# Optimization experiments

Measured on AMD Instinct MI355X. Metric: run time of the kernel, lower is better.

## Reference

```python
import jax, jax.numpy as jnp
import numpy as np

SP, WD, H, HID = 8, 3, 8, 256
D = HID // H
TEMP = 0.1


def setup_inputs() -> dict:
    key = jax.random.key(0)
    ks = jax.random.split(key, 14)
    B, Lq, Lk, F = 4, 1024, 2048, SP + WD
    s = 0.05
    return {
        "q_fp": jax.random.normal(ks[0], (B, Lq, F), jnp.float32),
        "v_ret": jax.random.normal(ks[1], (B, Lk, F), jnp.float32),
        "pi_star": jax.random.uniform(ks[2], (B, Lq, Lk), jnp.float32),
        "Wq_s": jax.random.normal(ks[3], (HID, SP), jnp.float32) * s,
        "bq_s": jax.random.normal(ks[4], (HID,), jnp.float32) * s,
        "Wk_s": jax.random.normal(ks[5], (HID, SP), jnp.float32) * s,
        "bk_s": jax.random.normal(ks[6], (HID,), jnp.float32) * s,
        "Wq_w": jax.random.normal(ks[7], (HID, WD), jnp.float32) * s,
        "bq_w": jax.random.normal(ks[8], (HID,), jnp.float32) * s,
        "Wk_w": jax.random.normal(ks[9], (HID, WD), jnp.float32) * s,
        "bk_w": jax.random.normal(ks[10], (HID,), jnp.float32) * s,
        "Wv": jax.random.normal(ks[11], (HID, F), jnp.float32) * s,
        "bv": jnp.zeros((HID,), jnp.float32),
        "Wo": jax.random.normal(ks[12], (HID, HID), jnp.float32) * s,
        "bo": jnp.zeros((HID,), jnp.float32),
        "wave_blend": jnp.array(0.5, jnp.float32),
    }


def _proj(x, W, b):
    # x: [B, L, F_in] -> [B, H, L, D]
    B, L, _ = x.shape
    return (x @ W.T + b).reshape(B, L, H, D).transpose(0, 2, 1, 3)


def reference(q_fp, v_ret, pi_star, Wq_s, bq_s, Wk_s, bk_s, Wq_w, bq_w, Wk_w, bk_w, Wv, bv, Wo, bo, wave_blend):
    B, Lq, _ = q_fp.shape
    # split streams: first SP dims spatial, next WD dims wave (F == SP+WD)
    q_sp, q_wv = q_fp[..., :SP], q_fp[..., SP:SP + WD]
    k_sp, k_wv = v_ret[..., :SP], v_ret[..., SP:SP + WD]
    # structural branch: scaled dot product
    q_struct = _proj(q_sp, Wq_s, bq_s)
    k_struct = _proj(k_sp, Wk_s, bk_s)
    spatial_logits = jnp.einsum('bhqd,bhkd->bhqk', q_struct, k_struct) / np.float32(np.sqrt(D))
    # wave branch: negative squared euclidean distance via norm expansion
    q_wp = _proj(q_wv, Wq_w, bq_w)
    k_wp = _proj(k_wv, Wk_w, bk_w)
    qn = jnp.sum(q_wp * q_wp, axis=-1)[..., :, None]   # [B,H,Lq,1]
    kn = jnp.sum(k_wp * k_wp, axis=-1)[..., None, :]   # [B,H,1,Lk]
    qk = jnp.einsum('bhqd,bhkd->bhqk', q_wp, k_wp)
    wave_logits = -(qn + kn - 2.0 * qk) / np.float32(TEMP)
    alpha = jax.nn.sigmoid(wave_blend)
    transport_mask = jnp.log(jnp.clip(pi_star, 1e-9, None))[:, None]  # [B,1,Lq,Lk]
    attn = jax.nn.softmax((1.0 - alpha) * spatial_logits + alpha * wave_logits + transport_mask, axis=-1)
    values = _proj(v_ret, Wv, bv)  # [B,H,Lk,D]
    ctx = jnp.einsum('bhqk,bhkd->bhqd', attn, values)
    ctx = ctx.transpose(0, 2, 1, 3).reshape(B, Lq, HID)
    return ctx @ Wo.T + bo
```

## Files before the change

kernel.cpp:

```cpp
#include <hip/hip_runtime.h>
#include <hip/hip_bf16.h>
#include <cstdint>

#define B_    4
#define LQ    1024
#define LK    2048
#define FEAT  11
#define SP_   8
#define WD_   3
#define H_    8
#define HID_  256
#define LOG2E 1.4426950408889634f
#define SPLIT 2
#define KPS   (LK / SPLIT)
#define ITERS (KPS / 64)

typedef __attribute__((ext_vector_type(4))) float f32x4;
typedef __attribute__((ext_vector_type(8))) short bf16x8;
typedef __attribute__((ext_vector_type(4))) short s16x4;

__device__ __forceinline__ float sigmoidf_(float x) { return 1.f / (1.f + __expf(-x)); }

__device__ __forceinline__ short f2bf(float f) {
  unsigned u = __float_as_uint(f);
  u += 0x7fffu + ((u >> 16) & 1u);
  return (short)(u >> 16);
}
__device__ __forceinline__ float bf2f(short s) {
  return __uint_as_float(((unsigned)(unsigned short)s) << 16);
}

__device__ __forceinline__ void gl_lds16(const void* g, void* l) {
  __builtin_amdgcn_global_load_lds(
      (const __attribute__((address_space(1))) unsigned int*)g,
      (__attribute__((address_space(3))) unsigned int*)l, 16, 0, 0);
}

__global__ __launch_bounds__(256) void proj_q_kernel(
    const float* __restrict__ q_fp, const float* __restrict__ Wq_s,
    const float* __restrict__ bq_s, const float* __restrict__ Wq_w,
    const float* __restrict__ bq_w, const float* __restrict__ wb,
    short* __restrict__ Qh)
{
  const int row = blockIdx.x;
  const int t   = threadIdx.x;
  const float alpha = sigmoidf_(wb[0]);
  const float c1 = (1.f - alpha) * 0.17677669529663687f * LOG2E;
  const float c2 = 2.f * alpha * 10.f * LOG2E;

  const float* x = q_fp + (size_t)row * FEAT;
  float xs[FEAT];
  #pragma unroll
  for (int f = 0; f < FEAT; ++f) xs[f] = x[f];

  float s = bq_s[t];
  #pragma unroll
  for (int f = 0; f < SP_; ++f) s += xs[f] * Wq_s[t * SP_ + f];
  float w = bq_w[t];
  #pragma unroll
  for (int f = 0; f < WD_; ++f) w += xs[SP_ + f] * Wq_w[t * WD_ + f];

  const int h = t >> 5, d = t & 31;
  const int b = row >> 10, q = row & (LQ - 1);
  const size_t base = ((size_t)(b * H_ + h) * LQ + q) * 64;
  Qh[base + d]      = f2bf(c1 * s);
  Qh[base + 32 + d] = f2bf(c2 * w);
}

__global__ __launch_bounds__(256) void projk_pack_kernel(
    const float* __restrict__ v_ret, const float* __restrict__ Wk_s,
    const float* __restrict__ bk_s, const float* __restrict__ Wk_w,
    const float* __restrict__ bk_w, const float* __restrict__ Wv,
    const float* __restrict__ bv,   const float* __restrict__ wb,
    short* __restrict__ KV, float* __restrict__ kb)
{
  __shared__ float ldsv[64][33];
  const int blk = blockIdx.x, bh = blockIdx.y;
  const int b = bh >> 3, h = bh & 7;
  const int t = threadIdx.x;
  const int kl = t >> 2, part = t & 3;
  const int k = blk * 64 + kl;
  const float alpha = sigmoidf_(wb[0]);

  const float* x = v_ret + (size_t)(b * LK + k) * FEAT;
  float xs[FEAT];
  #pragma unroll
  for (int f = 0; f < FEAT; ++f) xs[f] = x[f];

  float s8[8], w8[8], v8[8];
  #pragma unroll
  for (int i = 0; i < 8; ++i) {
    const int d = h * 32 + part * 8 + i;
    float s = bk_s[d];
    #pragma unroll
    for (int f = 0; f < SP_; ++f) s += xs[f] * Wk_s[d * SP_ + f];
    float w = bk_w[d];
    #pragma unroll
    for (int f = 0; f < WD_; ++f) w += xs[SP_ + f] * Wk_w[d * WD_ + f];
    float v = bv[d];
    #pragma unroll
    for (int f = 0; f < FEAT; ++f) v += xs[f] * Wv[d * FEAT + f];
    s8[i] = s; w8[i] = w; v8[i] = v;
    ldsv[kl][part * 8 + i] = v;
  }

  float sq = 0.f;
  #pragma unroll
  for (int i = 0; i < 8; ++i) sq += w8[i] * w8[i];
  sq += __shfl_xor(sq, 1);
  sq += __shfl_xor(sq, 2);
  if (part == 0) kb[(size_t)bh * LK + k] = -10.f * alpha * LOG2E * sq;

  const int a  = kl >> 5;
  const int bb = (kl >> 2) & 1;
  const int p  = kl - a * 32 - bb * 4;
  const int lo = ((p >> 3) << 2) | (p & 3);
  const int t4 = a * 2 + bb;
  const size_t base = ((size_t)bh * 32 + blk) * 768;

  bf16x8 hs, hw;
  #pragma unroll
  for (int i = 0; i < 8; ++i) { hs[i] = f2bf(s8[i]); hw[i] = f2bf(w8[i]); }
  *(bf16x8*)(KV + (base + (t4 * 2 + 0) * 64 + part * 16 + lo) * 8) = hs;
  *(bf16x8*)(KV + (base + (t4 * 2 + 1) * 64 + part * 16 + lo) * 8) = hw;

  __syncthreads();

  {
    const int j = t >> 6, l = t & 63;
    const int dt = j >> 1, kw = j & 1;
    const int lo2 = l & 15, quad = l >> 4;
    const int d = dt * 16 + lo2;
    bf16x8 hv;
    #pragma unroll
    for (int i = 0; i < 8; ++i)
      hv[i] = f2bf(ldsv[kw * 32 + quad * 8 + i][d]);
    *(bf16x8*)(KV + (base + 512 + t) * 8) = hv;
  }
}

__global__ __launch_bounds__(256) void pi_prepack_kernel(
    const float* __restrict__ pi, float* __restrict__ piP)
{
  const int Gid = blockIdx.x * 256 + threadIdx.x;
  const int g    = Gid & 255;
  const int kblk = (Gid >> 8) & 31;
  const int qt   = (Gid >> 13) & 63;
  const int b    = Gid >> 19;
  const int t4 = g >> 6, l = g & 63;
  const int lo = l & 15, quad = l >> 4;
  const int q = qt * 16 + lo;
  const int k = kblk * 64 + ((t4 >> 1) << 5) + ((t4 & 1) << 2) + quad * 8;
  const f32x4 v = *(const f32x4*)(pi + ((size_t)(b * LQ + q) * LK + k));
  *(f32x4*)(piP + (size_t)Gid * 4) = v;
}

union PF { int i[4]; bf16x8 v; };

__global__ __launch_bounds__(256, 4) void attn_kernel(
    const short* __restrict__ Qh, const short* __restrict__ KV,
    const float* __restrict__ kb, const float* __restrict__ piP,
    float* __restrict__ part)
{
  __shared__ short skv[2][6144];
  const int bh = blockIdx.y;
  const int sp = blockIdx.z;
  const int b = bh >> 3;
  const int wv = threadIdx.x >> 6;
  const int lane = threadIdx.x & 63;
  const int lo16 = lane & 15;
  const int quad = lane >> 4;
  const int q = blockIdx.x * 64 + wv * 16 + lo16;
  const int qt = blockIdx.x * 4 + wv;
  const int k0 = sp * KPS;
  const int blk0 = sp * 16;

  const size_t qoff = ((size_t)bh * LQ + q) * 64 + quad * 8;
  const bf16x8 qh0 = *(const bf16x8*)(Qh + qoff);
  const bf16x8 qh1 = *(const bf16x8*)(Qh + qoff + 32);

  const float* pibase = piP + (((size_t)(b * 64 + qt) * 32 + blk0) << 10) + lane * 4;
  const float* kbbase = kb + (size_t)bh * LK + k0 + quad * 8;

  float m = -1e30f, l = 0.f;
  f32x4 o0 = {0.f, 0.f, 0.f, 0.f}, o1 = {0.f, 0.f, 0.f, 0.f};

  {
    const size_t gb = ((size_t)bh * 32 + blk0) * 768;
    #pragma unroll
    for (int c = 0; c < 3; ++c)
      gl_lds16(KV + (gb + c * 256 + wv * 64 + lane) * 8,
               &skv[0][c * 2048 + wv * 512]);
  }

  #pragma unroll 2
  for (int it = 0; it < ITERS; ++it) {
    __syncthreads();
    if (it + 1 < ITERS) {
      const size_t gb = ((size_t)bh * 32 + blk0 + it + 1) * 768;
      short* db = skv[(it + 1) & 1];
      #pragma unroll
      for (int c = 0; c < 3; ++c)
        gl_lds16(KV + (gb + c * 256 + wv * 64 + lane) * 8,
                 db + c * 2048 + wv * 512);
    }
    const short* cbuf = skv[it & 1];

    const float* pp = pibase + (it << 10);
    f32x4 pi4[4];
    #pragma unroll
    for (int t4 = 0; t4 < 4; ++t4) pi4[t4] = *(const f32x4*)(pp + t4 * 256);
    const float* bp = kbbase + it * 64;
    f32x4 kb4[4];
    kb4[0] = *(const f32x4*)(bp);      kb4[1] = *(const f32x4*)(bp + 4);
    kb4[2] = *(const f32x4*)(bp + 32); kb4[3] = *(const f32x4*)(bp + 36);

    f32x4 st[4];
    #pragma unroll
    for (int t4 = 0; t4 < 4; ++t4) {
      const bf16x8 ka0 = *(const bf16x8*)(cbuf + ((t4 * 2 + 0) * 64 + lane) * 8);
      const bf16x8 ka1 = *(const bf16x8*)(cbuf + ((t4 * 2 + 1) * 64 + lane) * 8);
      f32x4 z = {0.f, 0.f, 0.f, 0.f};
      z = __builtin_amdgcn_mfma_f32_16x16x32_bf16(ka0, qh0, z, 0, 0, 0);
      z = __builtin_amdgcn_mfma_f32_16x16x32_bf16(ka1, qh1, z, 0, 0, 0);
      st[t4] = z;
    }

    float lg[16];
    #pragma unroll
    for (int t4 = 0; t4 < 4; ++t4) {
      #pragma unroll
      for (int r = 0; r < 4; ++r) lg[t4 * 4 + r] = st[t4][r] + kb4[t4][r];
    }

    float cm = lg[0];
    #pragma unroll
    for (int j = 1; j < 16; ++j) cm = fmaxf(cm, lg[j]);
    cm = fmaxf(cm, __shfl_xor(cm, 16));
    cm = fmaxf(cm, __shfl_xor(cm, 32));
    const float mn = fmaxf(m, cm);
    const float sc = __builtin_amdgcn_exp2f(m - mn);

    unsigned eu[16];
    #pragma unroll
    for (int t4 = 0; t4 < 4; ++t4) {
      #pragma unroll
      for (int r = 0; r < 4; ++r)
        eu[t4 * 4 + r] = __float_as_uint(
            __builtin_amdgcn_exp2f(lg[t4 * 4 + r] - mn) * fmaxf(pi4[t4][r], 1e-9f));
    }

    PF pf0, pf1;
    float ps = 0.f;
    #pragma unroll
    for (int p = 0; p < 4; ++p) {
      const int w0 = __builtin_amdgcn_perm(eu[2 * p + 1], eu[2 * p], 0x07060302u);
      const int w1 = __builtin_amdgcn_perm(eu[8 + 2 * p + 1], eu[8 + 2 * p], 0x07060302u);
      pf0.i[p] = w0; pf1.i[p] = w1;
      ps += __uint_as_float(((unsigned)w0) << 16) + __uint_as_float(w0 & 0xffff0000u);
      ps += __uint_as_float(((unsigned)w1) << 16) + __uint_as_float(w1 & 0xffff0000u);
    }
    ps += __shfl_xor(ps, 16);
    ps += __shfl_xor(ps, 32);
    l = l * sc + ps;
    m = mn;
    #pragma unroll
    for (int r = 0; r < 4; ++r) { o0[r] *= sc; o1[r] *= sc; }

    const bf16x8 va00 = *(const bf16x8*)(cbuf + ((512 + 0 * 64) + lane) * 8);
    const bf16x8 va01 = *(const bf16x8*)(cbuf + ((512 + 1 * 64) + lane) * 8);
    const bf16x8 va10 = *(const bf16x8*)(cbuf + ((512 + 2 * 64) + lane) * 8);
    const bf16x8 va11 = *(const bf16x8*)(cbuf + ((512 + 3 * 64) + lane) * 8);
    o0 = __builtin_amdgcn_mfma_f32_16x16x32_bf16(va00, pf0.v, o0, 0, 0, 0);
    o0 = __builtin_amdgcn_mfma_f32_16x16x32_bf16(va01, pf1.v, o0, 0, 0, 0);
    o1 = __builtin_amdgcn_mfma_f32_16x16x32_bf16(va10, pf0.v, o1, 0, 0, 0);
    o1 = __builtin_amdgcn_mfma_f32_16x16x32_bf16(va11, pf1.v, o1, 0, 0, 0);
  }

  float* ppart = part + ((size_t)(sp * 32 + bh) * LQ + q) * 36;
  if (quad == 0) { ppart[0] = m; ppart[1] = l; }
  *(f32x4*)(ppart + 4 + quad * 4)  = o0;
  *(f32x4*)(ppart + 20 + quad * 4) = o1;
}

__global__ __launch_bounds__(256) void wo_prep_kernel(
    const float* __restrict__ Wo, short* __restrict__ WoH, short* __restrict__ WoL)
{
  const int i = (blockIdx.x * 256 + threadIdx.x) * 4;
  const f32x4 v = *(const f32x4*)(Wo + i);
  s16x4 h, l;
  #pragma unroll
  for (int j = 0; j < 4; ++j) {
    h[j] = f2bf(v[j]);
    l[j] = f2bf(v[j] - bf2f(h[j]));
  }
  *(s16x4*)(WoH + i) = h;
  *(s16x4*)(WoL + i) = l;
}

__global__ __launch_bounds__(256) void out_kernel(
    const float* __restrict__ part, const short* __restrict__ WoH,
    const short* __restrict__ WoL, const float* __restrict__ bo,
    float* __restrict__ out)
{
  const int t = threadIdx.x;
  const int wv = t >> 6, lane = t & 63;
  const int lo16 = lane & 15, quad = lane >> 4;
  const int mt = blockIdx.x;
  const size_t gq = (size_t)mt * 16 + lo16;
  const int b = (int)(gq >> 10), qq = (int)(gq & (LQ - 1));

  bf16x8 Ah[8], Al[8];
  #pragma unroll
  for (int win = 0; win < 8; ++win) {
    const size_t r = (size_t)(b * H_ + win) * LQ + qq;
    const float* p0 = part + r * 36;
    const float* p1 = part + (r + (size_t)B_ * H_ * LQ) * 36;
    const float m0 = p0[0], l0 = p0[1], m1 = p1[0], l1 = p1[1];
    const float mM = fmaxf(m0, m1);
    const float w0 = __builtin_amdgcn_exp2f(m0 - mM);
    const float w1 = __builtin_amdgcn_exp2f(m1 - mM);
    const float inv = 1.f / (w0 * l0 + w1 * l1);
    const f32x4 a0  = *(const f32x4*)(p0 + 4 + quad * 8);
    const f32x4 a0b = *(const f32x4*)(p0 + 8 + quad * 8);
    const f32x4 a1  = *(const f32x4*)(p1 + 4 + quad * 8);
    const f32x4 a1b = *(const f32x4*)(p1 + 8 + quad * 8);
    float c8[8];
    #pragma unroll
    for (int j = 0; j < 4; ++j) {
      c8[j]     = (w0 * a0[j]  + w1 * a1[j])  * inv;
      c8[4 + j] = (w0 * a0b[j] + w1 * a1b[j]) * inv;
    }
    #pragma unroll
    for (int j = 0; j < 8; ++j) {
      const short hi = f2bf(c8[j]);
      Ah[win][j] = hi;
      Al[win][j] = f2bf(c8[j] - bf2f(hi));
    }
  }

  const int n0 = wv * 64;
  #pragma unroll
  for (int nt = 0; nt < 4; ++nt) {
    const int nb = n0 + nt * 16;
    const short* bh = WoH + (size_t)(nb + lo16) * HID_ + quad * 8;
    const short* bl = WoL + (size_t)(nb + lo16) * HID_ + quad * 8;
    const float bias = bo[nb + lo16];
    f32x4 acc = {bias, bias, bias, bias};
    #pragma unroll
    for (int win = 0; win < 8; ++win) {
      const bf16x8 Bh = *(const bf16x8*)(bh + win * 32);
      const bf16x8 Bl = *(const bf16x8*)(bl + win * 32);
      acc = __builtin_amdgcn_mfma_f32_16x16x32_bf16(Ah[win], Bh, acc, 0, 0, 0);
      acc = __builtin_amdgcn_mfma_f32_16x16x32_bf16(Al[win], Bh, acc, 0, 0, 0);
      acc = __builtin_amdgcn_mfma_f32_16x16x32_bf16(Ah[win], Bl, acc, 0, 0, 0);
    }
    #pragma unroll
    for (int r4 = 0; r4 < 4; ++r4)
      out[(size_t)(mt * 16 + quad * 4 + r4) * HID_ + nb + lo16] = acc[r4];
  }
}

extern "C" void kernel_launch(void* const* d_in, const int* in_sizes, int n_in,
                              void* d_out, int out_size, void* d_ws, size_t ws_size,
                              hipStream_t stream)
{
  const float* q_fp  = (const float*)d_in[0];
  const float* v_ret = (const float*)d_in[1];
  const float* pi    = (const float*)d_in[2];
  const float* Wq_s  = (const float*)d_in[3];
  const float* bq_s  = (const float*)d_in[4];
  const float* Wk_s  = (const float*)d_in[5];
  const float* bk_s  = (const float*)d_in[6];
  const float* Wq_w  = (const float*)d_in[7];
  const float* bq_w  = (const float*)d_in[8];
  const float* Wk_w  = (const float*)d_in[9];
  const float* bk_w  = (const float*)d_in[10];
  const float* Wv    = (const float*)d_in[11];
  const float* bv    = (const float*)d_in[12];
  const float* Wo    = (const float*)d_in[13];
  const float* bo    = (const float*)d_in[14];
  const float* wb    = (const float*)d_in[15];
  float* out = (float*)d_out;

  short* Qh   = (short*)d_ws;
  short* KV   = Qh + (size_t)2097152;
  float* kbuf = (float*)(KV + (size_t)6291456);
  float* piP  = kbuf + (size_t)65536;
  float* part = piP + (size_t)8388608;
  short* WoH  = (short*)piP;
  short* WoL  = WoH + (size_t)65536;

  proj_q_kernel<<<B_ * LQ, 256, 0, stream>>>(q_fp, Wq_s, bq_s, Wq_w, bq_w, wb, Qh);
  projk_pack_kernel<<<dim3(LK / 64, 32), 256, 0, stream>>>(
      v_ret, Wk_s, bk_s, Wk_w, bk_w, Wv, bv, wb, KV, kbuf);
  pi_prepack_kernel<<<8192, 256, 0, stream>>>(pi, piP);
  attn_kernel<<<dim3(LQ / 64, 32, SPLIT), 256, 0, stream>>>(Qh, KV, kbuf, piP, part);
  wo_prep_kernel<<<64, 256, 0, stream>>>(Wo, WoH, WoL);
  out_kernel<<<(B_ * LQ) / 16, 256, 0, stream>>>(part, WoH, WoL, bo, out);
}
```

Measured before the change: 179.1 us.

## Software-pipeline pi/kb loads with manual double-buffer unroll and remap grid to 1D

Restructures the attention loop into an explicit two-stage unroll: pi and key-bias values for the next step are loaded into registers while the current step computes, and LDS buffers are addressed statically. The grid becomes 1D with batch-head and split interleaved in the low bits of the block id, changing block scheduling order. The clamp on pi before multiplying is removed. Register pressure rises from the extra prefetched vectors, which may affect occupancy.

```diff
diff --git a/kernel.cpp b/kernel.cpp
--- a/kernel.cpp
+++ b/kernel.cpp
@@ -157,22 +157,91 @@
 
 union PF { int i[4]; bf16x8 v; };
 
+__device__ __forceinline__ void attn_step(
+    const short* __restrict__ cbuf, bf16x8 qh0, bf16x8 qh1,
+    const f32x4* __restrict__ pi4, const f32x4* __restrict__ kb4,
+    int lane, float& m, float& l, f32x4& o0, f32x4& o1)
+{
+  f32x4 st[4];
+  #pragma unroll
+  for (int t4 = 0; t4 < 4; ++t4) {
+    const bf16x8 ka0 = *(const bf16x8*)(cbuf + ((t4 * 2 + 0) * 64 + lane) * 8);
+    const bf16x8 ka1 = *(const bf16x8*)(cbuf + ((t4 * 2 + 1) * 64 + lane) * 8);
+    f32x4 z = {0.f, 0.f, 0.f, 0.f};
+    z = __builtin_amdgcn_mfma_f32_16x16x32_bf16(ka0, qh0, z, 0, 0, 0);
+    z = __builtin_amdgcn_mfma_f32_16x16x32_bf16(ka1, qh1, z, 0, 0, 0);
+    st[t4] = z;
+  }
+
+  float lg[16];
+  #pragma unroll
+  for (int t4 = 0; t4 < 4; ++t4) {
+    #pragma unroll
+    for (int r = 0; r < 4; ++r) lg[t4 * 4 + r] = st[t4][r] + kb4[t4][r];
+  }
+
+  float cm = lg[0];
+  #pragma unroll
+  for (int j = 1; j < 16; ++j) cm = fmaxf(cm, lg[j]);
+  cm = fmaxf(cm, __shfl_xor(cm, 16));
+  cm = fmaxf(cm, __shfl_xor(cm, 32));
+  const float mn = fmaxf(m, cm);
+  const float sc = __builtin_amdgcn_exp2f(m - mn);
+
+  unsigned eu[16];
+  #pragma unroll
+  for (int t4 = 0; t4 < 4; ++t4) {
+    #pragma unroll
+    for (int r = 0; r < 4; ++r)
+      eu[t4 * 4 + r] = __float_as_uint(
+          __builtin_amdgcn_exp2f(lg[t4 * 4 + r] - mn) * pi4[t4][r]);
+  }
+
+  PF pf0, pf1;
+  float ps = 0.f;
+  #pragma unroll
+  for (int p = 0; p < 4; ++p) {
+    const int w0 = __builtin_amdgcn_perm(eu[2 * p + 1], eu[2 * p], 0x07060302u);
+    const int w1 = __builtin_amdgcn_perm(eu[8 + 2 * p + 1], eu[8 + 2 * p], 0x07060302u);
+    pf0.i[p] = w0; pf1.i[p] = w1;
+    ps += __uint_as_float(((unsigned)w0) << 16) + __uint_as_float(w0 & 0xffff0000u);
+    ps += __uint_as_float(((unsigned)w1) << 16) + __uint_as_float(w1 & 0xffff0000u);
+  }
+  ps += __shfl_xor(ps, 16);
+  ps += __shfl_xor(ps, 32);
+  l = l * sc + ps;
+  m = mn;
+  #pragma unroll
+  for (int r = 0; r < 4; ++r) { o0[r] *= sc; o1[r] *= sc; }
+
+  const bf16x8 va00 = *(const bf16x8*)(cbuf + ((512 + 0 * 64) + lane) * 8);
+  const bf16x8 va01 = *(const bf16x8*)(cbuf + ((512 + 1 * 64) + lane) * 8);
+  const bf16x8 va10 = *(const bf16x8*)(cbuf + ((512 + 2 * 64) + lane) * 8);
+  const bf16x8 va11 = *(const bf16x8*)(cbuf + ((512 + 3 * 64) + lane) * 8);
+  o0 = __builtin_amdgcn_mfma_f32_16x16x32_bf16(va00, pf0.v, o0, 0, 0, 0);
+  o0 = __builtin_amdgcn_mfma_f32_16x16x32_bf16(va01, pf1.v, o0, 0, 0, 0);
+  o1 = __builtin_amdgcn_mfma_f32_16x16x32_bf16(va10, pf0.v, o1, 0, 0, 0);
+  o1 = __builtin_amdgcn_mfma_f32_16x16x32_bf16(va11, pf1.v, o1, 0, 0, 0);
+}
+
 __global__ __launch_bounds__(256, 4) void attn_kernel(
     const short* __restrict__ Qh, const short* __restrict__ KV,
     const float* __restrict__ kb, const float* __restrict__ piP,
     float* __restrict__ part)
 {
   __shared__ short skv[2][6144];
-  const int bh = blockIdx.y;
-  const int sp = blockIdx.z;
+  const int id = blockIdx.x;
+  const int combo = id & 63;
+  const int qblk  = id >> 6;
+  const int bh = combo >> 1;
+  const int sp = combo & 1;
   const int b = bh >> 3;
   const int wv = threadIdx.x >> 6;
   const int lane = threadIdx.x & 63;
   const int lo16 = lane & 15;
   const int quad = lane >> 4;
-  const int q = blockIdx.x * 64 + wv * 16 + lo16;
-  const int qt = blockIdx.x * 4 + wv;
-  const int k0 = sp * KPS;
+  const int q  = qblk * 64 + wv * 16 + lo16;
+  const int qt = qblk * 4 + wv;
   const int blk0 = sp * 16;
 
   const size_t qoff = ((size_t)bh * LQ + q) * 64 + quad * 8;
@@ -180,7 +249,7 @@
   const bf16x8 qh1 = *(const bf16x8*)(Qh + qoff + 32);
 
   const float* pibase = piP + (((size_t)(b * 64 + qt) * 32 + blk0) << 10) + lane * 4;
-  const float* kbbase = kb + (size_t)bh * LK + k0 + quad * 8;
+  const float* kbbase = kb + (size_t)bh * LK + sp * KPS + quad * 8;
 
   float m = -1e30f, l = 0.f;
   f32x4 o0 = {0.f, 0.f, 0.f, 0.f}, o1 = {0.f, 0.f, 0.f, 0.f};
@@ -193,89 +262,46 @@
                &skv[0][c * 2048 + wv * 512]);
   }
 
-  #pragma unroll 2
-  for (int it = 0; it < ITERS; ++it) {
+  f32x4 piA[4], kbA[4], piB[4], kbB[4];
+#define PI_LOAD(PID, KBD, IT) do {                                   \
+    const float* pp_ = pibase + ((size_t)(IT) << 10);                \
+    PID[0] = *(const f32x4*)(pp_);                                   \
+    PID[1] = *(const f32x4*)(pp_ + 256);                             \
+    PID[2] = *(const f32x4*)(pp_ + 512);                             \
+    PID[3] = *(const f32x4*)(pp_ + 768);                             \
+    const float* bp_ = kbbase + (IT) * 64;                           \
+    KBD[0] = *(const f32x4*)(bp_);                                   \
+    KBD[1] = *(const f32x4*)(bp_ + 4);                               \
+    KBD[2] = *(const f32x4*)(bp_ + 32);                              \
+    KBD[3] = *(const f32x4*)(bp_ + 36);                              \
+  } while (0)
+
+  PI_LOAD(piA, kbA, 0);
+
+  for (int it = 0; it < ITERS; it += 2) {
     __syncthreads();
-    if (it + 1 < ITERS) {
+    {
       const size_t gb = ((size_t)bh * 32 + blk0 + it + 1) * 768;
-      short* db = skv[(it + 1) & 1];
       #pragma unroll
       for (int c = 0; c < 3; ++c)
         gl_lds16(KV + (gb + c * 256 + wv * 64 + lane) * 8,
-                 db + c * 2048 + wv * 512);
+                 &skv[1][c * 2048 + wv * 512]);
     }
-    const short* cbuf = skv[it & 1];
-
-    const float* pp = pibase + (it << 10);
-    f32x4 pi4[4];
-    #pragma unroll
-    for (int t4 = 0; t4 < 4; ++t4) pi4[t4] = *(const f32x4*)(pp + t4 * 256);
-    const float* bp = kbbase + it * 64;
-    f32x4 kb4[4];
-    kb4[0] = *(const f32x4*)(bp);      kb4[1] = *(const f32x4*)(bp + 4);
-    kb4[2] = *(const f32x4*)(bp + 32); kb4[3] = *(const f32x4*)(bp + 36);
-
-    f32x4 st[4];
-    #pragma unroll
-    for (int t4 = 0; t4 < 4; ++t4) {
-      const bf16x8 ka0 = *(const bf16x8*)(cbuf + ((t4 * 2 + 0) * 64 + lane) * 8);
-      const bf16x8 ka1 = *(const bf16x8*)(cbuf + ((t4 * 2 + 1) * 64 + lane) * 8);
-      f32x4 z = {0.f, 0.f, 0.f, 0.f};
-      z = __builtin_amdgcn_mfma_f32_16x16x32_bf16(ka0, qh0, z, 0, 0, 0);
-      z = __builtin_amdgcn_mfma_f32_16x16x32_bf16(ka1, qh1, z, 0, 0, 0);
-      st[t4] = z;
+    PI_LOAD(piB, kbB, it + 1);
+    attn_step(skv[0], qh0, qh1, piA, kbA, lane, m, l, o0, o1);
+
+    __syncthreads();
+    if (it + 2 < ITERS) {
+      const size_t gb = ((size_t)bh * 32 + blk0 + it + 2) * 768;
+      #pragma unroll
+      for (int c = 0; c < 3; ++c)
+        gl_lds16(KV + (gb + c * 256 + wv * 64 + lane) * 8,
+                 &skv[0][c * 2048 + wv * 512]);
+      PI_LOAD(piA, kbA, it + 2);
     }
-
-    float lg[16];
-    #pragma unroll
-    for (int t4 = 0; t4 < 4; ++t4) {
-      #pragma unroll
-      for (int r = 0; r < 4; ++r) lg[t4 * 4 + r] = st[t4][r] + kb4[t4][r];
-    }
-
-    float cm = lg[0];
-    #pragma unroll
-    for (int j = 1; j < 16; ++j) cm = fmaxf(cm, lg[j]);
-    cm = fmaxf(cm, __shfl_xor(cm, 16));
-    cm = fmaxf(cm, __shfl_xor(cm, 32));
-    const float mn = fmaxf(m, cm);
-    const float sc = __builtin_amdgcn_exp2f(m - mn);
-
-    unsigned eu[16];
-    #pragma unroll
-    for (int t4 = 0; t4 < 4; ++t4) {
-      #pragma unroll
-      for (int r = 0; r < 4; ++r)
-        eu[t4 * 4 + r] = __float_as_uint(
-            __builtin_amdgcn_exp2f(lg[t4 * 4 + r] - mn) * fmaxf(pi4[t4][r], 1e-9f));
-    }
-
-    PF pf0, pf1;
-    float ps = 0.f;
-    #pragma unroll
-    for (int p = 0; p < 4; ++p) {
-      const int w0 = __builtin_amdgcn_perm(eu[2 * p + 1], eu[2 * p], 0x07060302u);
-      const int w1 = __builtin_amdgcn_perm(eu[8 + 2 * p + 1], eu[8 + 2 * p], 0x07060302u);
-      pf0.i[p] = w0; pf1.i[p] = w1;
-      ps += __uint_as_float(((unsigned)w0) << 16) + __uint_as_float(w0 & 0xffff0000u);
-      ps += __uint_as_float(((unsigned)w1) << 16) + __uint_as_float(w1 & 0xffff0000u);
-    }
-    ps += __shfl_xor(ps, 16);
-    ps += __shfl_xor(ps, 32);
-    l = l * sc + ps;
-    m = mn;
-    #pragma unroll
-    for (int r = 0; r < 4; ++r) { o0[r] *= sc; o1[r] *= sc; }
-
-    const bf16x8 va00 = *(const bf16x8*)(cbuf + ((512 + 0 * 64) + lane) * 8);
-    const bf16x8 va01 = *(const bf16x8*)(cbuf + ((512 + 1 * 64) + lane) * 8);
-    const bf16x8 va10 = *(const bf16x8*)(cbuf + ((512 + 2 * 64) + lane) * 8);
-    const bf16x8 va11 = *(const bf16x8*)(cbuf + ((512 + 3 * 64) + lane) * 8);
-    o0 = __builtin_amdgcn_mfma_f32_16x16x32_bf16(va00, pf0.v, o0, 0, 0, 0);
-    o0 = __builtin_amdgcn_mfma_f32_16x16x32_bf16(va01, pf1.v, o0, 0, 0, 0);
-    o1 = __builtin_amdgcn_mfma_f32_16x16x32_bf16(va10, pf0.v, o1, 0, 0, 0);
-    o1 = __builtin_amdgcn_mfma_f32_16x16x32_bf16(va11, pf1.v, o1, 0, 0, 0);
-  }
+    attn_step(skv[1], qh0, qh1, piB, kbB, lane, m, l, o0, o1);
+  }
+#undef PI_LOAD
 
   float* ppart = part + ((size_t)(sp * 32 + bh) * LQ + q) * 36;
   if (quad == 0) { ppart[0] = m; ppart[1] = l; }
@@ -395,7 +421,7 @@
   projk_pack_kernel<<<dim3(LK / 64, 32), 256, 0, stream>>>(
       v_ret, Wk_s, bk_s, Wk_w, bk_w, Wv, bv, wb, KV, kbuf);
   pi_prepack_kernel<<<8192, 256, 0, stream>>>(pi, piP);
-  attn_kernel<<<dim3(LQ / 64, 32, SPLIT), 256, 0, stream>>>(Qh, KV, kbuf, piP, part);
+  attn_kernel<<<(LQ / 64) * 32 * SPLIT, 256, 0, stream>>>(Qh, KV, kbuf, piP, part);
   wo_prep_kernel<<<64, 256, 0, stream>>>(Wo, WoH, WoL);
   out_kernel<<<(B_ * LQ) / 16, 256, 0, stream>>>(part, WoH, WoL, bo, out);
 }
```

New measurement: 177.5 us. About the same (-0.9%).
